# Kernel tuning notes

Measured on AMD Instinct MI355X. Metric: run time of the kernel, lower is better.

Reference implementation:

```python
import jax, jax.numpy as jnp
import numpy as np

I = 32   # input_dim
H = 64   # hidden_dim


def setup_inputs() -> dict:
    key = jax.random.key(0)
    k_seq, k_wi, k_wh, k_bi, k_bh = jax.random.split(key, 5)
    B, T = 4096, 512
    s = 1.0 / np.sqrt(H)  # PyTorch GRU init range
    return {
        "seq": jax.random.normal(k_seq, (B, T, I), dtype=jnp.float32),
        "W_ih": jax.random.uniform(k_wi, (3 * H, I), minval=-s, maxval=s, dtype=jnp.float32),
        "W_hh": jax.random.uniform(k_wh, (3 * H, H), minval=-s, maxval=s, dtype=jnp.float32),
        "b_ih": jax.random.uniform(k_bi, (3 * H,), minval=-s, maxval=s, dtype=jnp.float32),
        "b_hh": jax.random.uniform(k_bh, (3 * H,), minval=-s, maxval=s, dtype=jnp.float32),
    }


def reference(seq, W_ih, W_hh, b_ih, b_hh):
    # Single-layer GRU (PyTorch gate ordering r, z, n); returns final hidden state (B, H).
    B, T, _ = seq.shape
    # Precompute input projections for all timesteps: (B, T, 3H) -> scan over T.
    x_proj = jnp.einsum('bti,gi->btg', seq, W_ih) + b_ih  # g = 3H
    x_proj = jnp.moveaxis(x_proj, 1, 0)  # (T, B, 3H)

    def step(h, xp):
        hp = h @ W_hh.T + b_hh  # (B, 3H)
        xr, xz, xn = jnp.split(xp, 3, axis=-1)
        hr, hz, hn = jnp.split(hp, 3, axis=-1)
        r = jax.nn.sigmoid(xr + hr)
        z = jax.nn.sigmoid(xz + hz)
        n = jnp.tanh(xn + r * hn)
        h_new = (1.0 - z) * n + z * h
        return h_new, None

    h0 = jnp.zeros((B, H), dtype=seq.dtype)
    h_final, _ = jax.lax.scan(step, h0, x_proj)
    return h_final
```

## Files before the change

### kernel.cpp

```cpp
#include <hip/hip_runtime.h>


#define TSTEPS 512
#define IDIM 32
#define HDIM 64

typedef __bf16 bf16x8 __attribute__((ext_vector_type(8)));
typedef __bf16 bf16x4 __attribute__((ext_vector_type(4)));
typedef float f32x4 __attribute__((ext_vector_type(4)));

#define NLOG2E -1.4426950408889634f
#define TWOLOG2E 2.8853900817779268f

#define LOADPAIR(dst0, dst1, ptr, off)                                     \
    asm volatile("global_load_dwordx4 %0, %2, off offset:%c3\n\t"          \
                 "global_load_dwordx4 %1, %2, off offset:%c4"              \
        : "=&v"(dst0), "=&v"(dst1)                                         \
        : "v"(ptr), "i"(off), "i"((off) + 16));

#define ISSUE_CHUNK(qq, baseT) do {                                        \
    const float* _p = seqRow + (size_t)(baseT) * IDIM;                     \
    LOADPAIR(qq[0][0], qq[0][1], _p, 0)                                    \
    LOADPAIR(qq[1][0], qq[1][1], _p, 128)                                  \
    LOADPAIR(qq[2][0], qq[2][1], _p, 256)                                  \
    LOADPAIR(qq[3][0], qq[3][1], _p, 384)                                  \
    LOADPAIR(qq[4][0], qq[4][1], _p, 512)                                  \
    LOADPAIR(qq[5][0], qq[5][1], _p, 640)                                  \
    LOADPAIR(qq[6][0], qq[6][1], _p, 768)                                  \
    LOADPAIR(qq[7][0], qq[7][1], _p, 896)                                  \
} while (0)

#define WAITDEP(qq)                                                        \
    asm volatile("s_waitcnt vmcnt(0)"                                      \
        : "+v"(qq[0][0]), "+v"(qq[0][1]), "+v"(qq[1][0]), "+v"(qq[1][1]), \
          "+v"(qq[2][0]), "+v"(qq[2][1]), "+v"(qq[3][0]), "+v"(qq[3][1]), \
          "+v"(qq[4][0]), "+v"(qq[4][1]), "+v"(qq[5][0]), "+v"(qq[5][1]), \
          "+v"(qq[6][0]), "+v"(qq[6][1]), "+v"(qq[7][0]), "+v"(qq[7][1]))

#define WG_BARRIER() do {                                                  \
    asm volatile("s_waitcnt lgkmcnt(0)" ::: "memory");                     \
    __builtin_amdgcn_s_barrier();                                          \
} while (0)

__global__ __launch_bounds__(256, 1) void gru_fused_kernel(
    const float* __restrict__ seq, const float* __restrict__ W_ih,
    const float* __restrict__ W_hh, const float* __restrict__ b_ih,
    const float* __restrict__ b_hh, float* __restrict__ out)
{
    __shared__ __bf16 hB[2][16][72];

    const int tid  = threadIdx.x;
    const int w    = tid >> 6;
    const int lane = tid & 63;
    const int l    = lane & 15;
    const int q    = lane >> 4;
    const int b0   = blockIdx.x * 16;

    for (int i = tid; i < 2 * 16 * 72; i += 256)
        (&hB[0][0][0])[i] = (__bf16)0.0f;

    bf16x8 aH[3][2], aI[3];
    #pragma unroll
    for (int g = 0; g < 3; ++g) {
        const float scl = (g < 2) ? NLOG2E : 1.0f;
        const int row = g * 64 + w * 16 + l;
        #pragma unroll
        for (int kc = 0; kc < 2; ++kc) {
            const float* p = W_hh + row * HDIM + kc * 32 + q * 8;
            #pragma unroll
            for (int j = 0; j < 8; ++j) aH[g][kc][j] = (__bf16)(scl * p[j]);
        }
        const float* pi = W_ih + row * IDIM + q * 8;
        #pragma unroll
        for (int j = 0; j < 8; ++j) aI[g][j] = (__bf16)(scl * pi[j]);
    }

    f32x4 biasR4, biasZ4, biasXN4, biasHN4;
    #pragma unroll
    for (int r = 0; r < 4; ++r) {
        const int g = w * 16 + 4 * q + r;
        biasR4[r]  = NLOG2E * (b_ih[g]      + b_hh[g]);
        biasZ4[r]  = NLOG2E * (b_ih[64 + g] + b_hh[64 + g]);
        biasXN4[r] = b_ih[128 + g];
        biasHN4[r] = b_hh[128 + g];
    }

    float h[4] = {0.f, 0.f, 0.f, 0.f};

    const float* seqRow = seq + ((size_t)(b0 + l) * TSTEPS) * IDIM + q * 8;

    f32x4 qA[8][2], qB[8][2];
    ISSUE_CHUNK(qA, 0);
    ISSUE_CHUNK(qB, 8);
    WAITDEP(qA);
    WAITDEP(qB);

    WG_BARRIER();

    bf16x8 xb;
    #pragma unroll
    for (int j = 0; j < 4; ++j) {
        xb[j]     = (__bf16)qA[0][0][j];
        xb[4 + j] = (__bf16)qA[0][1][j];
    }
    f32x4 accR  = __builtin_amdgcn_mfma_f32_16x16x32_bf16(aI[0], xb, biasR4, 0, 0, 0);
    f32x4 accZ  = __builtin_amdgcn_mfma_f32_16x16x32_bf16(aI[1], xb, biasZ4, 0, 0, 0);
    f32x4 accXN = __builtin_amdgcn_mfma_f32_16x16x32_bf16(aI[2], xb, biasXN4, 0, 0, 0);

    for (int tc = 0; tc < TSTEPS; tc += 16) {
        #pragma unroll
        for (int s = 0; s < 16; ++s) {
            const int buf = s & 1;

            bf16x8 hb0 = *(const bf16x8*)&hB[buf][l][q * 8];
            bf16x8 hb1 = *(const bf16x8*)&hB[buf][l][32 + q * 8];

            accR = __builtin_amdgcn_mfma_f32_16x16x32_bf16(aH[0][0], hb0, accR, 0, 0, 0);
            accR = __builtin_amdgcn_mfma_f32_16x16x32_bf16(aH[0][1], hb1, accR, 0, 0, 0);
            accZ = __builtin_amdgcn_mfma_f32_16x16x32_bf16(aH[1][0], hb0, accZ, 0, 0, 0);
            accZ = __builtin_amdgcn_mfma_f32_16x16x32_bf16(aH[1][1], hb1, accZ, 0, 0, 0);
            f32x4 accHN = __builtin_amdgcn_mfma_f32_16x16x32_bf16(aH[2][0], hb0, biasHN4, 0, 0, 0);
            accHN = __builtin_amdgcn_mfma_f32_16x16x32_bf16(aH[2][1], hb1, accHN, 0, 0, 0);

            bf16x4 hOut;
            #pragma unroll
            for (int r = 0; r < 4; ++r) {
                const float rg = __builtin_amdgcn_rcpf(1.0f + __builtin_amdgcn_exp2f(accR[r]));
                const float zg = __builtin_amdgcn_rcpf(1.0f + __builtin_amdgcn_exp2f(accZ[r]));
                const float v  = accXN[r] + rg * accHN[r];
                const float u  = __builtin_amdgcn_exp2f(TWOLOG2E * v);
                const float ng = 1.0f - 2.0f * __builtin_amdgcn_rcpf(1.0f + u);
                h[r] = ng + zg * (h[r] - ng);
                hOut[r] = (__bf16)h[r];
            }
            *(bf16x4*)&hB[buf ^ 1][l][w * 16 + 4 * q] = hOut;

            if (s == 7) {
                WAITDEP(qB);
                if (tc + 16 < TSTEPS) ISSUE_CHUNK(qA, tc + 16);
            }
            if (s == 15) {
                WAITDEP(qA);
                if (tc + 24 < TSTEPS) ISSUE_CHUNK(qB, tc + 24);
            }

            {
                const int s1 = s + 1;
                const f32x4* x0 = (s1 < 8) ? &qA[s1 & 7][0]
                                           : (s1 < 16) ? &qB[s1 & 7][0]
                                                       : &qA[0][0];
                bf16x8 xb1;
                #pragma unroll
                for (int j = 0; j < 4; ++j) {
                    xb1[j]     = (__bf16)x0[0][j];
                    xb1[4 + j] = (__bf16)x0[1][j];
                }
                accR  = __builtin_amdgcn_mfma_f32_16x16x32_bf16(aI[0], xb1, biasR4, 0, 0, 0);
                accZ  = __builtin_amdgcn_mfma_f32_16x16x32_bf16(aI[1], xb1, biasZ4, 0, 0, 0);
                accXN = __builtin_amdgcn_mfma_f32_16x16x32_bf16(aI[2], xb1, biasXN4, 0, 0, 0);
            }

            WG_BARRIER();
        }
    }

    float4 o = {h[0], h[1], h[2], h[3]};
    *(float4*)&out[(size_t)(b0 + l) * HDIM + w * 16 + 4 * q] = o;
}

extern "C" void kernel_launch(void* const* d_in, const int* in_sizes, int n_in,
                              void* d_out, int out_size, void* d_ws, size_t ws_size,
                              hipStream_t stream) {
    const float* seq  = (const float*)d_in[0];
    const float* W_ih = (const float*)d_in[1];
    const float* W_hh = (const float*)d_in[2];
    const float* b_ih = (const float*)d_in[3];
    const float* b_hh = (const float*)d_in[4];
    float* out = (float*)d_out;
    gru_fused_kernel<<<256, 256, 0, stream>>>(seq, W_ih, W_hh, b_ih, b_hh, out);
}
```

Before: 483.2 us.

## Split each hidden slice across two waves to halve the per-step gate epilogue

Doubles the workgroup to 512 threads. Each pair of waves computes the same MFMA tile redundantly, and each wave then evaluates the gate nonlinearities for only two of the four accumulator rows, halving the transcendental epilogue on the serial recurrence path. The input prefetch chunks shrink from 8 to 4 timesteps to reduce per-wave register pressure. The cost is duplicated MFMA and global-load work and a barrier over more waves.

```diff
diff --git a/kernel.cpp b/kernel.cpp
--- a/kernel.cpp
+++ b/kernel.cpp
@@ -6,8 +6,9 @@
 #define HDIM 64
 
 typedef __bf16 bf16x8 __attribute__((ext_vector_type(8)));
-typedef __bf16 bf16x4 __attribute__((ext_vector_type(4)));
+typedef __bf16 bf16x2 __attribute__((ext_vector_type(2)));
 typedef float f32x4 __attribute__((ext_vector_type(4)));
+typedef float f32x2 __attribute__((ext_vector_type(2)));
 
 #define NLOG2E -1.4426950408889634f
 #define TWOLOG2E 2.8853900817779268f
@@ -24,25 +25,42 @@
     LOADPAIR(qq[1][0], qq[1][1], _p, 128)                                  \
     LOADPAIR(qq[2][0], qq[2][1], _p, 256)                                  \
     LOADPAIR(qq[3][0], qq[3][1], _p, 384)                                  \
-    LOADPAIR(qq[4][0], qq[4][1], _p, 512)                                  \
-    LOADPAIR(qq[5][0], qq[5][1], _p, 640)                                  \
-    LOADPAIR(qq[6][0], qq[6][1], _p, 768)                                  \
-    LOADPAIR(qq[7][0], qq[7][1], _p, 896)                                  \
 } while (0)
 
 #define WAITDEP(qq)                                                        \
     asm volatile("s_waitcnt vmcnt(0)"                                      \
         : "+v"(qq[0][0]), "+v"(qq[0][1]), "+v"(qq[1][0]), "+v"(qq[1][1]), \
-          "+v"(qq[2][0]), "+v"(qq[2][1]), "+v"(qq[3][0]), "+v"(qq[3][1]), \
-          "+v"(qq[4][0]), "+v"(qq[4][1]), "+v"(qq[5][0]), "+v"(qq[5][1]), \
-          "+v"(qq[6][0]), "+v"(qq[6][1]), "+v"(qq[7][0]), "+v"(qq[7][1]))
+          "+v"(qq[2][0]), "+v"(qq[2][1]), "+v"(qq[3][0]), "+v"(qq[3][1]))
 
 #define WG_BARRIER() do {                                                  \
     asm volatile("s_waitcnt lgkmcnt(0)" ::: "memory");                     \
     __builtin_amdgcn_s_barrier();                                          \
 } while (0)
 
-__global__ __launch_bounds__(256, 1) void gru_fused_kernel(
+#define EPILOG(R0, R1, hPtr) do {                                          \
+    bf16x2 hOut;                                                           \
+    {                                                                      \
+        const float rg = __builtin_amdgcn_rcpf(1.0f + __builtin_amdgcn_exp2f(accR[R0])); \
+        const float zg = __builtin_amdgcn_rcpf(1.0f + __builtin_amdgcn_exp2f(accZ[R0])); \
+        const float v  = accXN[R0] + rg * accHN[R0];                       \
+        const float u  = __builtin_amdgcn_exp2f(TWOLOG2E * v);             \
+        const float ng = 1.0f - 2.0f * __builtin_amdgcn_rcpf(1.0f + u);    \
+        h[0] = ng + zg * (h[0] - ng);                                      \
+        hOut[0] = (__bf16)h[0];                                            \
+    }                                                                      \
+    {                                                                      \
+        const float rg = __builtin_amdgcn_rcpf(1.0f + __builtin_amdgcn_exp2f(accR[R1])); \
+        const float zg = __builtin_amdgcn_rcpf(1.0f + __builtin_amdgcn_exp2f(accZ[R1])); \
+        const float v  = accXN[R1] + rg * accHN[R1];                       \
+        const float u  = __builtin_amdgcn_exp2f(TWOLOG2E * v);             \
+        const float ng = 1.0f - 2.0f * __builtin_amdgcn_rcpf(1.0f + u);    \
+        h[1] = ng + zg * (h[1] - ng);                                      \
+        hOut[1] = (__bf16)h[1];                                            \
+    }                                                                      \
+    *(bf16x2*)(hPtr) = hOut;                                               \
+} while (0)
+
+__global__ __launch_bounds__(512, 2) void gru_fused_kernel(
     const float* __restrict__ seq, const float* __restrict__ W_ih,
     const float* __restrict__ W_hh, const float* __restrict__ b_ih,
     const float* __restrict__ b_hh, float* __restrict__ out)
@@ -51,19 +69,21 @@
 
     const int tid  = threadIdx.x;
     const int w    = tid >> 6;
+    const int hw   = w >> 1;
+    const int sub  = w & 1;
     const int lane = tid & 63;
     const int l    = lane & 15;
     const int q    = lane >> 4;
     const int b0   = blockIdx.x * 16;
 
-    for (int i = tid; i < 2 * 16 * 72; i += 256)
+    for (int i = tid; i < 2 * 16 * 72; i += 512)
         (&hB[0][0][0])[i] = (__bf16)0.0f;
 
     bf16x8 aH[3][2], aI[3];
     #pragma unroll
     for (int g = 0; g < 3; ++g) {
         const float scl = (g < 2) ? NLOG2E : 1.0f;
-        const int row = g * 64 + w * 16 + l;
+        const int row = g * 64 + hw * 16 + l;
         #pragma unroll
         for (int kc = 0; kc < 2; ++kc) {
             const float* p = W_hh + row * HDIM + kc * 32 + q * 8;
@@ -78,20 +98,20 @@
     f32x4 biasR4, biasZ4, biasXN4, biasHN4;
     #pragma unroll
     for (int r = 0; r < 4; ++r) {
-        const int g = w * 16 + 4 * q + r;
+        const int g = hw * 16 + 4 * q + r;
         biasR4[r]  = NLOG2E * (b_ih[g]      + b_hh[g]);
         biasZ4[r]  = NLOG2E * (b_ih[64 + g] + b_hh[64 + g]);
         biasXN4[r] = b_ih[128 + g];
         biasHN4[r] = b_hh[128 + g];
     }
 
-    float h[4] = {0.f, 0.f, 0.f, 0.f};
+    float h[2] = {0.f, 0.f};
 
     const float* seqRow = seq + ((size_t)(b0 + l) * TSTEPS) * IDIM + q * 8;
 
-    f32x4 qA[8][2], qB[8][2];
+    f32x4 qA[4][2], qB[4][2];
     ISSUE_CHUNK(qA, 0);
-    ISSUE_CHUNK(qB, 8);
+    ISSUE_CHUNK(qB, 4);
     WAITDEP(qA);
     WAITDEP(qB);
 
@@ -107,9 +127,11 @@
     f32x4 accZ  = __builtin_amdgcn_mfma_f32_16x16x32_bf16(aI[1], xb, biasZ4, 0, 0, 0);
     f32x4 accXN = __builtin_amdgcn_mfma_f32_16x16x32_bf16(aI[2], xb, biasXN4, 0, 0, 0);
 
-    for (int tc = 0; tc < TSTEPS; tc += 16) {
+    __bf16* const hWr = &hB[0][0][0] + l * 72 + hw * 16 + 4 * q + 2 * sub;
+
+    for (int tc = 0; tc < TSTEPS; tc += 8) {
         #pragma unroll
-        for (int s = 0; s < 16; ++s) {
+        for (int s = 0; s < 8; ++s) {
             const int buf = s & 1;
 
             bf16x8 hb0 = *(const bf16x8*)&hB[buf][l][q * 8];
@@ -122,33 +144,23 @@
             f32x4 accHN = __builtin_amdgcn_mfma_f32_16x16x32_bf16(aH[2][0], hb0, biasHN4, 0, 0, 0);
             accHN = __builtin_amdgcn_mfma_f32_16x16x32_bf16(aH[2][1], hb1, accHN, 0, 0, 0);
 
-            bf16x4 hOut;
-            #pragma unroll
-            for (int r = 0; r < 4; ++r) {
-                const float rg = __builtin_amdgcn_rcpf(1.0f + __builtin_amdgcn_exp2f(accR[r]));
-                const float zg = __builtin_amdgcn_rcpf(1.0f + __builtin_amdgcn_exp2f(accZ[r]));
-                const float v  = accXN[r] + rg * accHN[r];
-                const float u  = __builtin_amdgcn_exp2f(TWOLOG2E * v);
-                const float ng = 1.0f - 2.0f * __builtin_amdgcn_rcpf(1.0f + u);
-                h[r] = ng + zg * (h[r] - ng);
-                hOut[r] = (__bf16)h[r];
+            __bf16* hp = hWr + (buf ^ 1) * (16 * 72);
+            if (sub == 0) { EPILOG(0, 1, hp); } else { EPILOG(2, 3, hp); }
+
+            if (s == 3) {
+                WAITDEP(qB);
+                if (tc + 8 < TSTEPS) ISSUE_CHUNK(qA, tc + 8);
             }
-            *(bf16x4*)&hB[buf ^ 1][l][w * 16 + 4 * q] = hOut;
-
             if (s == 7) {
-                WAITDEP(qB);
-                if (tc + 16 < TSTEPS) ISSUE_CHUNK(qA, tc + 16);
-            }
-            if (s == 15) {
                 WAITDEP(qA);
-                if (tc + 24 < TSTEPS) ISSUE_CHUNK(qB, tc + 24);
+                if (tc + 12 < TSTEPS) ISSUE_CHUNK(qB, tc + 12);
             }
 
             {
                 const int s1 = s + 1;
-                const f32x4* x0 = (s1 < 8) ? &qA[s1 & 7][0]
-                                           : (s1 < 16) ? &qB[s1 & 7][0]
-                                                       : &qA[0][0];
+                const f32x4* x0 = (s1 < 4) ? &qA[s1 & 3][0]
+                                           : (s1 < 8) ? &qB[s1 & 3][0]
+                                                      : &qA[0][0];
                 bf16x8 xb1;
                 #pragma unroll
                 for (int j = 0; j < 4; ++j) {
@@ -164,8 +176,8 @@
         }
     }
 
-    float4 o = {h[0], h[1], h[2], h[3]};
-    *(float4*)&out[(size_t)(b0 + l) * HDIM + w * 16 + 4 * q] = o;
+    f32x2 o = {h[0], h[1]};
+    *(f32x2*)&out[(size_t)(b0 + l) * HDIM + hw * 16 + 4 * q + 2 * sub] = o;
 }
 
 extern "C" void kernel_launch(void* const* d_in, const int* in_sizes, int n_in,
@@ -177,5 +189,5 @@
     const float* b_ih = (const float*)d_in[3];
     const float* b_hh = (const float*)d_in[4];
     float* out = (float*)d_out;
-    gru_fused_kernel<<<256, 256, 0, stream>>>(seq, W_ih, W_hh, b_ih, b_hh, out);
+    gru_fused_kernel<<<256, 512, 0, stream>>>(seq, W_ih, W_hh, b_ih, b_hh, out);
 }
```

Result: slower. 641.5 us (+32.8%).
